# Performance work log

Hardware: AMD Instinct MI355X
Metric: run time of the kernel (lower is better)

## Reference

```python
import jax, jax.numpy as jnp
import numpy as np

B, G, A, C = 128, 16, 8732, 21
THR = 0.5        # overlap_threshold
NEG_POS = 3      # neg_pos_ratio
VAR0, VAR1 = 0.1, 0.2  # loc_variance


def center_to_point(b):
    cxcy, wh = b[:, :2], b[:, 2:]
    return jnp.concatenate([cxcy - wh / 2, cxcy + wh / 2], axis=-1)


def iou_matrix(a, b):
    # a: [G,4], b: [A,4] point coords (x1,y1,x2,y2) -> [G,A]
    tl = jnp.maximum(a[:, None, :2], b[None, :, :2])
    br = jnp.minimum(a[:, None, 2:], b[None, :, 2:])
    wh = jnp.clip(br - tl, 0.0)
    inter = wh[..., 0] * wh[..., 1]
    area_a = (a[:, 2] - a[:, 0]) * (a[:, 3] - a[:, 1])
    area_b = (b[:, 2] - b[:, 0]) * (b[:, 3] - b[:, 1])
    return inter / (area_a[:, None] + area_b[None, :] - inter)


def encode(anchors, gt_pt):
    # anchors [A,4] (cx,cy,w,h); gt_pt [A,4] point coords
    g_cxcy = (gt_pt[:, :2] + gt_pt[:, 2:]) / 2
    g_wh = gt_pt[:, 2:] - gt_pt[:, :2]
    d_cxcy = (g_cxcy - anchors[:, :2]) / (anchors[:, 2:] * VAR0)
    d_wh = jnp.log(g_wh / anchors[:, 2:]) / VAR1
    return jnp.concatenate([d_cxcy, d_wh], axis=-1)


def match(boxes, labels, anchors, anchors_pt):
    # boxes [G,4] point coords, labels [G] int
    iou = iou_matrix(boxes, anchors_pt)           # [G,A]
    anchor_index = jnp.argmax(iou, axis=1)        # best anchor per gt, [G]
    gt_overlap = jnp.max(iou, axis=0)             # best gt overlap per anchor, [A]
    gt_index = jnp.argmax(iou, axis=0)            # best gt per anchor, [A]
    gt_overlap = gt_overlap.at[anchor_index].set(1.0)
    for i in range(G):
        gt_index = gt_index.at[anchor_index[i]].set(i)
    gt_coords = boxes[gt_index]                   # [A,4]
    loc = encode(anchors, gt_coords)              # [A,4]
    conf = labels[gt_index] + 1                   # [A], 0 reserved for background
    conf = jnp.where(gt_overlap < THR, 0, conf)
    return loc, conf


def setup_inputs() -> dict:
    key = jax.random.key(0)
    k1, k2, k3, k4, k5, k6, k7 = jax.random.split(key, 7)
    predict_offset_coords = jax.random.normal(k1, (B, A, 4), jnp.float32)
    predict_confidences = jax.random.normal(k2, (B, A, C), jnp.float32)
    # valid gt boxes: centers in [0.2,0.8], sizes in [0.05,0.3]
    c = jax.random.uniform(k3, (B, G, 2)) * 0.6 + 0.2
    s = jax.random.uniform(k4, (B, G, 2)) * 0.25 + 0.05
    target_boxes = jnp.concatenate([c - s / 2, c + s / 2], axis=-1)
    target_labels = jax.random.randint(k5, (B, G), 0, C - 1).astype(jnp.int32)
    # anchors in center-coord form (cx,cy,w,h), strictly positive w,h
    acx = jax.random.uniform(k6, (A, 2)) * 0.9 + 0.05
    awh = jax.random.uniform(k7, (A, 2)) * 0.25 + 0.05
    anchors = jnp.concatenate([acx, awh], axis=-1)
    return {"predict_offset_coords": predict_offset_coords,
            "predict_confidences": predict_confidences,
            "target_boxes": target_boxes,
            "target_labels": target_labels,
            "anchors": anchors}


def reference(predict_offset_coords, predict_confidences, target_boxes, target_labels, anchors):
    anchors_pt = center_to_point(anchors)
    loc_t, conf_t = jax.vmap(match, in_axes=(0, 0, None, None))(
        target_boxes, target_labels, anchors, anchors_pt)
    # labels are built without grad in the original (fresh tensors)
    loc_t = jax.lax.stop_gradient(loc_t)
    conf_t = jax.lax.stop_gradient(conf_t)

    is_pos = conf_t > 0                            # [B,A]
    # smooth L1 (beta=1), summed over positive anchors
    diff = predict_offset_coords - loc_t
    ad = jnp.abs(diff)
    sl1 = jnp.where(ad < 1.0, 0.5 * diff * diff, ad - 0.5)
    loss_loc = jnp.sum(sl1 * is_pos[..., None])

    num_pos = jnp.sum(is_pos, axis=1, keepdims=True)      # [B,1]
    n_total = jnp.sum(num_pos).astype(jnp.float32)
    num_neg = jnp.minimum(NEG_POS * num_pos, A - 1)        # [B,1]

    logp = jax.nn.log_softmax(predict_confidences, axis=-1)
    nll = -jnp.take_along_axis(logp, conf_t[..., None], axis=-1)[..., 0]  # [B,A]

    # hard-negative mining via double argsort
    aux = jnp.where(is_pos, 0.0, nll)
    order = jnp.argsort(-aux, axis=1)
    rank = jnp.argsort(order, axis=1)
    is_neg = rank < num_neg

    sel = jnp.logical_or(is_pos, is_neg)
    loss_cls = jnp.sum(jnp.where(sel, nll, 0.0))
    return loss_loc / n_total, loss_cls / n_total
```

## Files before the change

### kernel.cpp

```cpp
#include <hip/hip_runtime.h>
#include <math.h>

#define B_ 128
#define G_ 16
#define A_ 8732
#define C_ 21
#define THR_ 0.5f
#define NEG_POS_ 3
#define VAR0_ 0.1f
#define VAR1_ 0.2f

#define BA_   (B_ * A_)
#define NTH_  (BA_ / 4)
#define NBLK_ ((NTH_ + 255) / 256)

#define MTPB_ 768
#define MNW_  (MTPB_ / 64)

struct Accum { float loss_loc; float loss_cls; int done; int pad; };

__global__ __launch_bounds__(MTPB_) void k_match(
    const float* __restrict__ tboxes,
    const int*   __restrict__ tlabels,
    const float* __restrict__ anchors,
    int*         __restrict__ match,
    int*         __restrict__ num_pos,
    Accum*                    acc)
{
    const int b    = blockIdx.x;
    const int tid  = threadIdx.x;
    const int lane = tid & 63;
    const int w    = tid >> 6;

    if (b == 0 && tid == 0) {
        acc->loss_loc = 0.f;
        acc->loss_cls = 0.f;
        acc->done     = 0;
    }

    __shared__ float         s_ov[A_];
    __shared__ unsigned char s_gi[A_];
    __shared__ float s_boxlds[G_ * 4];
    __shared__ int   s_lab[G_];
    __shared__ unsigned long long s_gb[MNW_ * G_];
    __shared__ int   s_forced[G_];
    __shared__ int   s_cnt[MNW_];

    if (tid < G_ * 4) s_boxlds[tid] = tboxes[b * G_ * 4 + tid];
    if (tid < G_)     s_lab[tid]    = tlabels[b * G_ + tid];
    __syncthreads();

    float bx0[G_], by0[G_], bx1[G_], by1[G_], bar[G_];
    #pragma unroll
    for (int g = 0; g < G_; ++g) {
        bx0[g] = s_boxlds[g * 4 + 0];
        by0[g] = s_boxlds[g * 4 + 1];
        bx1[g] = s_boxlds[g * 4 + 2];
        by1[g] = s_boxlds[g * 4 + 3];
        bar[g] = (bx1[g] - bx0[g]) * (by1[g] - by0[g]);
    }

    unsigned long long gb[G_];
    #pragma unroll
    for (int g = 0; g < G_; ++g) gb[g] = 0ull;

    for (int a = tid; a < A_; a += MTPB_) {
        float4 an = ((const float4*)anchors)[a];
        float ax0 = an.x - an.z * 0.5f, ay0 = an.y - an.w * 0.5f;
        float ax1 = an.x + an.z * 0.5f, ay1 = an.y + an.w * 0.5f;
        float area_b = (ax1 - ax0) * (ay1 - ay0);
        float bov = -1.f; int bg = 0;
        #pragma unroll
        for (int g = 0; g < G_; ++g) {
            float tlx = fmaxf(bx0[g], ax0);
            float tly = fmaxf(by0[g], ay0);
            float brx = fminf(bx1[g], ax1);
            float bry = fminf(by1[g], ay1);
            float wdt = fmaxf(brx - tlx, 0.f);
            float hgt = fmaxf(bry - tly, 0.f);
            float inter = wdt * hgt;
            float iou = inter / (bar[g] + area_b - inter);
            if (iou > bov) { bov = iou; bg = g; }
            unsigned long long pk =
                ((unsigned long long)__float_as_uint(iou) << 32) |
                (unsigned)(~(unsigned)a);
            if (pk > gb[g]) gb[g] = pk;
        }
        s_ov[a] = bov;
        s_gi[a] = (unsigned char)bg;
    }

    #pragma unroll
    for (int g = 0; g < G_; ++g) {
        #pragma unroll
        for (int off = 32; off > 0; off >>= 1) {
            unsigned long long o = __shfl_down(gb[g], off);
            if (o > gb[g]) gb[g] = o;
        }
    }
    if (lane == 0) {
        #pragma unroll
        for (int g = 0; g < G_; ++g) s_gb[w * G_ + g] = gb[g];
    }
    __syncthreads();
    if (tid < G_) {
        unsigned long long m = 0ull;
        #pragma unroll
        for (int wv = 0; wv < MNW_; ++wv) {
            unsigned long long v = s_gb[wv * G_ + tid];
            if (v > m) m = v;
        }
        s_forced[tid] = (int)(~(unsigned)(m & 0xFFFFFFFFull));
    }
    __syncthreads();
    if (tid == 0) {
        for (int g = 0; g < G_; ++g) {
            int a = s_forced[g];
            s_ov[a] = 1.0f;
            s_gi[a] = (unsigned char)g;
        }
    }
    __syncthreads();

    int cnt = 0;
    for (int a = tid; a < A_; a += MTPB_) {
        float ov = s_ov[a];
        int g = s_gi[a];
        int conf = (ov < THR_) ? 0 : (s_lab[g] + 1);
        match[b * A_ + a] = conf | (g << 8);
        cnt += (conf > 0);
    }
    #pragma unroll
    for (int off = 32; off > 0; off >>= 1) cnt += __shfl_down(cnt, off);
    if (lane == 0) s_cnt[w] = cnt;
    __syncthreads();
    if (tid == 0) {
        int t = 0;
        #pragma unroll
        for (int wv = 0; wv < MNW_; ++wv) t += s_cnt[wv];
        num_pos[b] = t;
    }
}

__global__ __launch_bounds__(256) void k_loss(
    const float* __restrict__ pred_off,
    const float* __restrict__ pred_conf,
    const float* __restrict__ tboxes,
    const float* __restrict__ anchors,
    const int*   __restrict__ match,
    float*       __restrict__ aux,
    Accum*                    acc)
{
    const int tid  = threadIdx.x;
    const int t    = blockIdx.x * 256 + tid;
    const int lane = tid & 63;
    const int w    = tid >> 6;

    __shared__ float s_lloc[4];
    __shared__ float s_pnll[4];

    float lloc = 0.f, pnll = 0.f;

    if (t < NTH_) {
        const float4* cp = (const float4*)pred_conf + (size_t)t * 21;
        float xx[84];
        #pragma unroll
        for (int k = 0; k < 21; ++k) {
            float4 v = cp[k];
            xx[4 * k + 0] = v.x; xx[4 * k + 1] = v.y;
            xx[4 * k + 2] = v.z; xx[4 * k + 3] = v.w;
        }
        int4 mk = ((const int4*)match)[t];
        int mkv[4]; mkv[0] = mk.x; mkv[1] = mk.y; mkv[2] = mk.z; mkv[3] = mk.w;
        float auxv[4];

        #pragma unroll
        for (int j = 0; j < 4; ++j) {
            const int base = 21 * j;
            float m = xx[base];
            #pragma unroll
            for (int c = 1; c < C_; ++c) m = fmaxf(m, xx[base + c]);
            float s = 0.f;
            #pragma unroll
            for (int c = 0; c < C_; ++c) s += __expf(xx[base + c] - m);
            float lse = m + __logf(s);

            int conf = mkv[j] & 0xff;
            int g    = mkv[j] >> 8;
            float xc = xx[base];
            #pragma unroll
            for (int c = 1; c < C_; ++c) xc = (conf == c) ? xx[base + c] : xc;
            float nll = lse - xc;
            bool pos = conf > 0;
            auxv[j] = pos ? 0.f : nll;

            if (pos) {
                pnll += nll;
                int i = t * 4 + j;
                int b = i / A_;
                int a = i - b * A_;
                float4 an = ((const float4*)anchors)[a];
                float4 bx = ((const float4*)tboxes)[b * G_ + g];
                float gcx = (bx.x + bx.z) * 0.5f, gcy = (bx.y + bx.w) * 0.5f;
                float gw = bx.z - bx.x, gh = bx.w - bx.y;
                float l0 = (gcx - an.x) / (an.z * VAR0_);
                float l1 = (gcy - an.y) / (an.w * VAR0_);
                float l2 = logf(gw / an.z) / VAR1_;
                float l3 = logf(gh / an.w) / VAR1_;
                float4 p = ((const float4*)pred_off)[i];
                float d, ad;
                d = p.x - l0; ad = fabsf(d); lloc += (ad < 1.f) ? 0.5f * d * d : ad - 0.5f;
                d = p.y - l1; ad = fabsf(d); lloc += (ad < 1.f) ? 0.5f * d * d : ad - 0.5f;
                d = p.z - l2; ad = fabsf(d); lloc += (ad < 1.f) ? 0.5f * d * d : ad - 0.5f;
                d = p.w - l3; ad = fabsf(d); lloc += (ad < 1.f) ? 0.5f * d * d : ad - 0.5f;
            }
        }
        ((float4*)aux)[t] = make_float4(auxv[0], auxv[1], auxv[2], auxv[3]);
    }

    #pragma unroll
    for (int off = 32; off > 0; off >>= 1) {
        lloc += __shfl_down(lloc, off);
        pnll += __shfl_down(pnll, off);
    }
    if (lane == 0) { s_lloc[w] = lloc; s_pnll[w] = pnll; }
    __syncthreads();
    if (tid == 0) {
        float L = s_lloc[0] + s_lloc[1] + s_lloc[2] + s_lloc[3];
        float P = s_pnll[0] + s_pnll[1] + s_pnll[2] + s_pnll[3];
        if (L != 0.f) atomicAdd(&acc->loss_loc, L);
        if (P != 0.f) atomicAdd(&acc->loss_cls, P);
    }
}

#define NPT_ 35
__global__ __launch_bounds__(256) void k_select(
    const float* __restrict__ aux,
    const int*   __restrict__ num_pos,
    Accum*                    acc,
    float*       __restrict__ out)
{
    const int b    = blockIdx.x;
    const int tid  = threadIdx.x;
    const int lane = tid & 63;
    const int w    = tid >> 6;

    __shared__ int   s_c[2][4];
    __shared__ int   s_cf[4];
    __shared__ float s_sf[4];
    __shared__ int   s_last;

    unsigned u[NPT_];
    #pragma unroll
    for (int j = 0; j < NPT_; ++j) {
        int a = tid + j * 256;
        u[j] = (a < A_) ? __float_as_uint(aux[(size_t)b * A_ + a]) : 0u;
    }

    const int K = min(NEG_POS_ * num_pos[b], A_ - 1);

    unsigned lo = 0u, hi = 0x7f800000u;
    int it = 0;
    while (lo < hi) {
        unsigned mid = (lo + hi) >> 1;
        int c = 0;
        #pragma unroll
        for (int j = 0; j < NPT_; ++j) c += (u[j] > mid);
        #pragma unroll
        for (int off = 32; off > 0; off >>= 1) c += __shfl_down(c, off);
        if (lane == 0) s_c[it & 1][w] = c;
        __syncthreads();
        int total = s_c[it & 1][0] + s_c[it & 1][1] + s_c[it & 1][2] + s_c[it & 1][3];
        if (total >= K) lo = mid + 1; else hi = mid;
        ++it;
    }

    int c = 0; float sm = 0.f;
    #pragma unroll
    for (int j = 0; j < NPT_; ++j) {
        if (u[j] > lo) { c++; sm += __uint_as_float(u[j]); }
    }
    #pragma unroll
    for (int off = 32; off > 0; off >>= 1) {
        c  += __shfl_down(c, off);
        sm += __shfl_down(sm, off);
    }
    if (lane == 0) { s_cf[w] = c; s_sf[w] = sm; }
    __syncthreads();
    if (tid == 0) {
        int   ct = s_cf[0] + s_cf[1] + s_cf[2] + s_cf[3];
        float st = s_sf[0] + s_sf[1] + s_sf[2] + s_sf[3];
        float T = __uint_as_float(lo);
        atomicAdd(&acc->loss_cls, st + (float)(K - ct) * T);
        __threadfence();
        int prev = atomicAdd(&acc->done, 1);
        s_last = (prev == B_ - 1) ? 1 : 0;
    }
    __syncthreads();

    if (s_last) {
        int n = (tid < B_) ? num_pos[tid] : 0;
        #pragma unroll
        for (int off = 32; off > 0; off >>= 1) n += __shfl_down(n, off);
        if (lane == 0) s_cf[w] = n;
        __syncthreads();
        if (tid == 0) {
            float nt = (float)(s_cf[0] + s_cf[1]);
            float L  = atomicAdd(&acc->loss_loc, 0.f);
            float Cc = atomicAdd(&acc->loss_cls, 0.f);
            out[0] = L / nt;
            out[1] = Cc / nt;
        }
    }
}

extern "C" void kernel_launch(void* const* d_in, const int* in_sizes, int n_in,
                              void* d_out, int out_size, void* d_ws, size_t ws_size,
                              hipStream_t stream) {
    const float* pred_off  = (const float*)d_in[0];
    const float* pred_conf = (const float*)d_in[1];
    const float* tboxes    = (const float*)d_in[2];
    const int*   tlabels   = (const int*)  d_in[3];
    const float* anchors   = (const float*)d_in[4];
    float* out = (float*)d_out;

    char* ws = (char*)d_ws;
    int*   match_ws = (int*)ws;     ws += (size_t)BA_ * sizeof(int);
    float* aux_ws   = (float*)ws;   ws += (size_t)BA_ * sizeof(float);
    int*   npos_ws  = (int*)ws;     ws += (size_t)((B_ + 3) & ~3) * sizeof(int);
    Accum* acc      = (Accum*)ws;

    k_match<<<B_, MTPB_, 0, stream>>>(tboxes, tlabels, anchors, match_ws, npos_ws, acc);
    k_loss<<<NBLK_, 256, 0, stream>>>(pred_off, pred_conf, tboxes, anchors,
                                      match_ws, aux_ws, acc);
    k_select<<<B_, 256, 0, stream>>>(aux_ws, npos_ws, acc, out);
}
```

Baseline: 237.3 us.

## Parallelize anchor matching across a 2D grid and fuse forced-match resolution into loss

The matching kernel now launches one thread per anchor across a batch-by-anchor-chunk grid, instead of one large block per batch image. Per-ground-truth best anchors are reduced with wave shuffles and global 64-bit atomicMax. Forced-match overrides, label lookup and the positive count move into the loss kernel, which now indexes per batch. This removes the serial per-batch loop and the block-level sync phases, at the cost of a wider intermediate buffer, global atomics and an extra zeroing launch.

```diff
diff --git a/kernel.cpp b/kernel.cpp
--- a/kernel.cpp
+++ b/kernel.cpp
@@ -10,159 +10,119 @@
 #define VAR0_ 0.1f
 #define VAR1_ 0.2f
 
-#define BA_   (B_ * A_)
-#define NTH_  (BA_ / 4)
-#define NBLK_ ((NTH_ + 255) / 256)
-
-#define MTPB_ 768
-#define MNW_  (MTPB_ / 64)
+#define BA_    (B_ * A_)
+#define NGRPB_ (A_ / 4)
+#define MBLKX_ ((A_ + 255) / 256)
+#define LBLKX_ ((NGRPB_ + 255) / 256)
 
 struct Accum { float loss_loc; float loss_cls; int done; int pad; };
 
-__global__ __launch_bounds__(MTPB_) void k_match(
+#define ZERO_U32_ (2048 * 2 + 128 + 4)
+__global__ __launch_bounds__(256) void k_zero(unsigned int* z) {
+    for (int i = threadIdx.x; i < ZERO_U32_; i += 256) z[i] = 0u;
+}
+
+__global__ __launch_bounds__(256) void k_match(
     const float* __restrict__ tboxes,
-    const int*   __restrict__ tlabels,
     const float* __restrict__ anchors,
-    int*         __restrict__ match,
-    int*         __restrict__ num_pos,
-    Accum*                    acc)
+    unsigned long long* __restrict__ ovgi,
+    unsigned long long* __restrict__ wsGT)
 {
-    const int b    = blockIdx.x;
+    const int b    = blockIdx.y;
     const int tid  = threadIdx.x;
+    const int a    = blockIdx.x * 256 + tid;
     const int lane = tid & 63;
-    const int w    = tid >> 6;
-
-    if (b == 0 && tid == 0) {
-        acc->loss_loc = 0.f;
-        acc->loss_cls = 0.f;
-        acc->done     = 0;
-    }
-
-    __shared__ float         s_ov[A_];
-    __shared__ unsigned char s_gi[A_];
-    __shared__ float s_boxlds[G_ * 4];
-    __shared__ int   s_lab[G_];
-    __shared__ unsigned long long s_gb[MNW_ * G_];
-    __shared__ int   s_forced[G_];
-    __shared__ int   s_cnt[MNW_];
-
-    if (tid < G_ * 4) s_boxlds[tid] = tboxes[b * G_ * 4 + tid];
-    if (tid < G_)     s_lab[tid]    = tlabels[b * G_ + tid];
+
+    __shared__ float s_box[G_ * 4];
+    if (tid < G_ * 4) s_box[tid] = tboxes[b * G_ * 4 + tid];
     __syncthreads();
 
     float bx0[G_], by0[G_], bx1[G_], by1[G_], bar[G_];
     #pragma unroll
     for (int g = 0; g < G_; ++g) {
-        bx0[g] = s_boxlds[g * 4 + 0];
-        by0[g] = s_boxlds[g * 4 + 1];
-        bx1[g] = s_boxlds[g * 4 + 2];
-        by1[g] = s_boxlds[g * 4 + 3];
+        bx0[g] = s_box[g * 4 + 0];
+        by0[g] = s_box[g * 4 + 1];
+        bx1[g] = s_box[g * 4 + 2];
+        by1[g] = s_box[g * 4 + 3];
         bar[g] = (bx1[g] - bx0[g]) * (by1[g] - by0[g]);
     }
 
-    unsigned long long gb[G_];
-    #pragma unroll
-    for (int g = 0; g < G_; ++g) gb[g] = 0ull;
-
-    for (int a = tid; a < A_; a += MTPB_) {
-        float4 an = ((const float4*)anchors)[a];
-        float ax0 = an.x - an.z * 0.5f, ay0 = an.y - an.w * 0.5f;
-        float ax1 = an.x + an.z * 0.5f, ay1 = an.y + an.w * 0.5f;
-        float area_b = (ax1 - ax0) * (ay1 - ay0);
-        float bov = -1.f; int bg = 0;
-        #pragma unroll
-        for (int g = 0; g < G_; ++g) {
-            float tlx = fmaxf(bx0[g], ax0);
-            float tly = fmaxf(by0[g], ay0);
-            float brx = fminf(bx1[g], ax1);
-            float bry = fminf(by1[g], ay1);
-            float wdt = fmaxf(brx - tlx, 0.f);
-            float hgt = fmaxf(bry - tly, 0.f);
-            float inter = wdt * hgt;
-            float iou = inter / (bar[g] + area_b - inter);
-            if (iou > bov) { bov = iou; bg = g; }
-            unsigned long long pk =
-                ((unsigned long long)__float_as_uint(iou) << 32) |
-                (unsigned)(~(unsigned)a);
-            if (pk > gb[g]) gb[g] = pk;
+    const bool valid = (a < A_);
+    const int  aa    = valid ? a : (A_ - 1);
+    float4 an = ((const float4*)anchors)[aa];
+    float ax0 = an.x - an.z * 0.5f, ay0 = an.y - an.w * 0.5f;
+    float ax1 = an.x + an.z * 0.5f, ay1 = an.y + an.w * 0.5f;
+    float area_b = (ax1 - ax0) * (ay1 - ay0);
+
+    float bov = -1.f; int bg = 0;
+    #pragma unroll
+    for (int g = 0; g < G_; ++g) {
+        float tlx = fmaxf(bx0[g], ax0);
+        float tly = fmaxf(by0[g], ay0);
+        float brx = fminf(bx1[g], ax1);
+        float bry = fminf(by1[g], ay1);
+        float wdt = fmaxf(brx - tlx, 0.f);
+        float hgt = fmaxf(bry - tly, 0.f);
+        float inter = wdt * hgt;
+        float iou = inter / (bar[g] + area_b - inter);
+        if (iou > bov) { bov = iou; bg = g; }
+
+        unsigned long long pk = valid
+            ? ((unsigned long long)__float_as_uint(iou) << 32) |
+              (unsigned)(~(unsigned)a)
+            : 0ull;
+        #pragma unroll
+        for (int off = 32; off > 0; off >>= 1) {
+            unsigned long long o = __shfl_down(pk, off);
+            if (o > pk) pk = o;
         }
-        s_ov[a] = bov;
-        s_gi[a] = (unsigned char)bg;
-    }
-
-    #pragma unroll
-    for (int g = 0; g < G_; ++g) {
-        #pragma unroll
-        for (int off = 32; off > 0; off >>= 1) {
-            unsigned long long o = __shfl_down(gb[g], off);
-            if (o > gb[g]) gb[g] = o;
-        }
-    }
-    if (lane == 0) {
-        #pragma unroll
-        for (int g = 0; g < G_; ++g) s_gb[w * G_ + g] = gb[g];
-    }
-    __syncthreads();
-    if (tid < G_) {
-        unsigned long long m = 0ull;
-        #pragma unroll
-        for (int wv = 0; wv < MNW_; ++wv) {
-            unsigned long long v = s_gb[wv * G_ + tid];
-            if (v > m) m = v;
-        }
-        s_forced[tid] = (int)(~(unsigned)(m & 0xFFFFFFFFull));
-    }
-    __syncthreads();
-    if (tid == 0) {
-        for (int g = 0; g < G_; ++g) {
-            int a = s_forced[g];
-            s_ov[a] = 1.0f;
-            s_gi[a] = (unsigned char)g;
-        }
-    }
-    __syncthreads();
-
-    int cnt = 0;
-    for (int a = tid; a < A_; a += MTPB_) {
-        float ov = s_ov[a];
-        int g = s_gi[a];
-        int conf = (ov < THR_) ? 0 : (s_lab[g] + 1);
-        match[b * A_ + a] = conf | (g << 8);
-        cnt += (conf > 0);
-    }
-    #pragma unroll
-    for (int off = 32; off > 0; off >>= 1) cnt += __shfl_down(cnt, off);
-    if (lane == 0) s_cnt[w] = cnt;
-    __syncthreads();
-    if (tid == 0) {
-        int t = 0;
-        #pragma unroll
-        for (int wv = 0; wv < MNW_; ++wv) t += s_cnt[wv];
-        num_pos[b] = t;
-    }
+        if (lane == 0)
+            atomicMax(&wsGT[b * G_ + g], pk);
+    }
+
+    if (valid)
+        ovgi[(size_t)b * A_ + a] =
+            ((unsigned long long)__float_as_uint(bov) << 32) | (unsigned)bg;
 }
 
 __global__ __launch_bounds__(256) void k_loss(
     const float* __restrict__ pred_off,
     const float* __restrict__ pred_conf,
     const float* __restrict__ tboxes,
+    const int*   __restrict__ tlabels,
     const float* __restrict__ anchors,
-    const int*   __restrict__ match,
+    const unsigned long long* __restrict__ ovgi,
+    const unsigned long long* __restrict__ wsGT,
     float*       __restrict__ aux,
+    int*         __restrict__ npos,
     Accum*                    acc)
 {
+    const int b    = blockIdx.y;
     const int tid  = threadIdx.x;
-    const int t    = blockIdx.x * 256 + tid;
+    const int gid  = blockIdx.x * 256 + tid;
     const int lane = tid & 63;
     const int w    = tid >> 6;
 
-    __shared__ float s_lloc[4];
-    __shared__ float s_pnll[4];
+    __shared__ int    s_win[G_];
+    __shared__ int    s_lab[G_];
+    __shared__ float4 s_bx[G_];
+    __shared__ float  s_lloc[4];
+    __shared__ float  s_pnll[4];
+    __shared__ int    s_cnt[4];
+
+    if (tid < G_) {
+        unsigned long long wv = wsGT[b * G_ + tid];
+        s_win[tid] = (int)(~(unsigned)(wv & 0xffffffffull));
+        s_lab[tid] = tlabels[b * G_ + tid];
+        s_bx[tid]  = ((const float4*)tboxes)[b * G_ + tid];
+    }
+    __syncthreads();
 
     float lloc = 0.f, pnll = 0.f;
-
-    if (t < NTH_) {
-        const float4* cp = (const float4*)pred_conf + (size_t)t * 21;
+    int   cnt  = 0;
+
+    if (gid < NGRPB_) {
+        const float4* cp = (const float4*)pred_conf + ((size_t)b * NGRPB_ + gid) * 21;
         float xx[84];
         #pragma unroll
         for (int k = 0; k < 21; ++k) {
@@ -170,13 +130,24 @@
             xx[4 * k + 0] = v.x; xx[4 * k + 1] = v.y;
             xx[4 * k + 2] = v.z; xx[4 * k + 3] = v.w;
         }
-        int4 mk = ((const int4*)match)[t];
-        int mkv[4]; mkv[0] = mk.x; mkv[1] = mk.y; mkv[2] = mk.z; mkv[3] = mk.w;
+        const ulonglong2* op = (const ulonglong2*)(ovgi + (size_t)b * A_) + gid * 2;
+        ulonglong2 o01 = op[0];
+        ulonglong2 o23 = op[1];
+        unsigned long long ovp[4] = { o01.x, o01.y, o23.x, o23.y };
         float auxv[4];
 
         #pragma unroll
-        for (int j = 0; j < 4; ++j) {
-            const int base = 21 * j;
+        for (int jj = 0; jj < 4; ++jj) {
+            const int base = 21 * jj;
+            const int a    = 4 * gid + jj;
+            float ov = __uint_as_float((unsigned)(ovp[jj] >> 32));
+            int   gi = (int)(ovp[jj] & 0xffull);
+            #pragma unroll
+            for (int g = 0; g < G_; ++g) {
+                if (s_win[g] == a) { ov = 1.0f; gi = g; }
+            }
+            int conf = (ov < THR_) ? 0 : (s_lab[gi] + 1);
+
             float m = xx[base];
             #pragma unroll
             for (int c = 1; c < C_; ++c) m = fmaxf(m, xx[base + c]);
@@ -185,29 +156,25 @@
             for (int c = 0; c < C_; ++c) s += __expf(xx[base + c] - m);
             float lse = m + __logf(s);
 
-            int conf = mkv[j] & 0xff;
-            int g    = mkv[j] >> 8;
             float xc = xx[base];
             #pragma unroll
             for (int c = 1; c < C_; ++c) xc = (conf == c) ? xx[base + c] : xc;
             float nll = lse - xc;
             bool pos = conf > 0;
-            auxv[j] = pos ? 0.f : nll;
+            auxv[jj] = pos ? 0.f : nll;
 
             if (pos) {
+                cnt++;
                 pnll += nll;
-                int i = t * 4 + j;
-                int b = i / A_;
-                int a = i - b * A_;
                 float4 an = ((const float4*)anchors)[a];
-                float4 bx = ((const float4*)tboxes)[b * G_ + g];
+                float4 bx = s_bx[gi];
                 float gcx = (bx.x + bx.z) * 0.5f, gcy = (bx.y + bx.w) * 0.5f;
                 float gw = bx.z - bx.x, gh = bx.w - bx.y;
                 float l0 = (gcx - an.x) / (an.z * VAR0_);
                 float l1 = (gcy - an.y) / (an.w * VAR0_);
                 float l2 = logf(gw / an.z) / VAR1_;
                 float l3 = logf(gh / an.w) / VAR1_;
-                float4 p = ((const float4*)pred_off)[i];
+                float4 p = ((const float4*)pred_off)[(size_t)b * A_ + a];
                 float d, ad;
                 d = p.x - l0; ad = fabsf(d); lloc += (ad < 1.f) ? 0.5f * d * d : ad - 0.5f;
                 d = p.y - l1; ad = fabsf(d); lloc += (ad < 1.f) ? 0.5f * d * d : ad - 0.5f;
@@ -215,21 +182,25 @@
                 d = p.w - l3; ad = fabsf(d); lloc += (ad < 1.f) ? 0.5f * d * d : ad - 0.5f;
             }
         }
-        ((float4*)aux)[t] = make_float4(auxv[0], auxv[1], auxv[2], auxv[3]);
+        ((float4*)(aux + (size_t)b * A_))[gid] =
+            make_float4(auxv[0], auxv[1], auxv[2], auxv[3]);
     }
 
     #pragma unroll
     for (int off = 32; off > 0; off >>= 1) {
         lloc += __shfl_down(lloc, off);
         pnll += __shfl_down(pnll, off);
-    }
-    if (lane == 0) { s_lloc[w] = lloc; s_pnll[w] = pnll; }
+        cnt  += __shfl_down(cnt, off);
+    }
+    if (lane == 0) { s_lloc[w] = lloc; s_pnll[w] = pnll; s_cnt[w] = cnt; }
     __syncthreads();
     if (tid == 0) {
         float L = s_lloc[0] + s_lloc[1] + s_lloc[2] + s_lloc[3];
         float P = s_pnll[0] + s_pnll[1] + s_pnll[2] + s_pnll[3];
+        int   Ct = s_cnt[0] + s_cnt[1] + s_cnt[2] + s_cnt[3];
         if (L != 0.f) atomicAdd(&acc->loss_loc, L);
         if (P != 0.f) atomicAdd(&acc->loss_cls, P);
+        if (Ct)       atomicAdd(&npos[b], Ct);
     }
 }
 
@@ -325,13 +296,25 @@
     float* out = (float*)d_out;
 
     char* ws = (char*)d_ws;
-    int*   match_ws = (int*)ws;     ws += (size_t)BA_ * sizeof(int);
-    float* aux_ws   = (float*)ws;   ws += (size_t)BA_ * sizeof(float);
-    int*   npos_ws  = (int*)ws;     ws += (size_t)((B_ + 3) & ~3) * sizeof(int);
-    Accum* acc      = (Accum*)ws;
-
-    k_match<<<B_, MTPB_, 0, stream>>>(tboxes, tlabels, anchors, match_ws, npos_ws, acc);
-    k_loss<<<NBLK_, 256, 0, stream>>>(pred_off, pred_conf, tboxes, anchors,
-                                      match_ws, aux_ws, acc);
+    unsigned long long* ovgi = (unsigned long long*)ws;
+    ws += (size_t)BA_ * sizeof(unsigned long long);
+    float* aux_ws = (float*)ws;
+    ws += (size_t)BA_ * sizeof(float);
+    unsigned long long* wsGT = (unsigned long long*)ws;
+    ws += (size_t)B_ * G_ * sizeof(unsigned long long);
+    int* npos_ws = (int*)ws;
+    ws += (size_t)B_ * sizeof(int);
+    Accum* acc = (Accum*)ws;
+
+    k_zero<<<1, 256, 0, stream>>>((unsigned int*)wsGT);
+    {
+        dim3 g(MBLKX_, B_);
+        k_match<<<g, 256, 0, stream>>>(tboxes, anchors, ovgi, wsGT);
+    }
+    {
+        dim3 g(LBLKX_, B_);
+        k_loss<<<g, 256, 0, stream>>>(pred_off, pred_conf, tboxes, tlabels, anchors,
+                                      ovgi, wsGT, aux_ws, npos_ws, acc);
+    }
     k_select<<<B_, 256, 0, stream>>>(aux_ws, npos_ws, acc, out);
 }
```

New measurement: 283.1 us. 1.19x slower.
